# Performance work log

Hardware: AMD Instinct MI355X
Metric: run time of the kernel (lower is better)

Reference implementation:

```python
import jax, jax.numpy as jnp
import numpy as np

C = 4096
C8 = C // 8  # 512, must equal h*w
B, H, W = 32, 16, 32


def setup_inputs() -> dict:
    key = jax.random.key(0)
    ks = jax.random.split(key, 8)
    s = 0.02
    return {
        "x": jax.random.normal(ks[0], (B, C, H, W), dtype=jnp.float32),
        "Wq": jax.random.normal(ks[1], (C8, C), dtype=jnp.float32) * s,
        "bq": jax.random.normal(ks[2], (C8,), dtype=jnp.float32) * s,
        "Wk": jax.random.normal(ks[3], (C8, C), dtype=jnp.float32) * s,
        "bk": jax.random.normal(ks[4], (C8,), dtype=jnp.float32) * s,
        "Wv": jax.random.normal(ks[5], (C, C), dtype=jnp.float32) * s,
        "bv": jax.random.normal(ks[6], (C,), dtype=jnp.float32) * s,
        "gamma": jax.random.normal(ks[7], (1,), dtype=jnp.float32),
    }


def reference(x, Wq, bq, Wk, bk, Wv, bv, gamma):
    b, c, h, w = x.shape
    xf = x.reshape(b, c, h * w)               # (b, c, hw)
    # 1x1 conv == per-position linear over channels
    q = jnp.einsum("oc,bcl->bol", Wq, xf) + bq[None, :, None]   # (b, c8, hw)
    k = jnp.einsum("oc,bcl->bol", Wk, xf) + bk[None, :, None]   # (b, c8, hw)
    v = jnp.einsum("oc,bcl->bol", Wv, xf) + bv[None, :, None]   # (b, c, hw)
    # energy = bmm(Q, K^T): (b, c8, c8); no sqrt(d) scaling (faithful)
    energy = jnp.einsum("bol,bpl->bop", q, k)
    attn = jax.nn.softmax(energy, axis=-1)
    # out = bmm(V, attn^T): out[b,c,p] = sum_k V[b,c,k] * attn[b,p,k]
    out = jnp.einsum("bck,bpk->bcp", v, attn)  # requires hw == c8
    out = out.reshape(b, c, h, w)
    return gamma * out + x
```

## Files before the change

kernel.cpp:

```cpp
#include <hip/hip_runtime.h>


typedef _Float16 f16;
typedef _Float16 h8 __attribute__((ext_vector_type(8)));
typedef _Float16 h4 __attribute__((ext_vector_type(4)));
typedef _Float16 h2 __attribute__((ext_vector_type(2)));
typedef float fx4 __attribute__((ext_vector_type(4)));

#define CC  4096
#define C8  512
#define HWD 512
#define NB  32

__device__ __forceinline__ h8 ldfragC(const char* s, int row, int cb) {
  const int b = ((row << 7) | cb) ^ ((row & 7) << 4);
  return *reinterpret_cast<const h8*>(s + b);
}

#define AS1C(p) ((const __attribute__((address_space(1))) unsigned int*)(p))
#define AS3(p)  ((__attribute__((address_space(3))) unsigned int*)(p))


#define STAGE_ALL(bufsel) { \
  char* la_ = smem + ((bufsel) << 16); \
  char* lb_ = la_ + 32768; \
  _Pragma("unroll") for (int q = 0; q < 4; ++q) { \
    __builtin_amdgcn_global_load_lds(AS1C(pA[q]), AS3(la_ + (q << 13) + w1024), 16, 0, 0); \
    __builtin_amdgcn_global_load_lds(AS1C(pB[q]), AS3(lb_ + (q << 13) + w1024), 16, 0, 0); \
    pA[q] += 128; pB[q] += 128; } }

#define STAGE2(bufsel, q) { \
  char* la_ = smem + ((bufsel) << 16); \
  char* lb_ = la_ + 32768; \
  __builtin_amdgcn_global_load_lds(AS1C(pA[q]), AS3(la_ + ((q) << 13) + w1024), 16, 0, 0); \
  __builtin_amdgcn_global_load_lds(AS1C(pB[q]), AS3(lb_ + ((q) << 13) + w1024), 16, 0, 0); \
  pA[q] += 128; pB[q] += 128; }

#define DSREADS_A(dst, hm, kh) \
  _Pragma("unroll") for (int f = 0; f < 4; ++f) \
    dst[f] = ldfragC(At, wr * 128 + (hm) * 64 + f * 16 + frow, (kh) * 64 + kq);

#define DSREADS_B(dst, kh) \
  _Pragma("unroll") for (int g = 0; g < 4; ++g) \
    dst[g] = ldfragC(Bt, wc * 64 + g * 16 + frow, (kh) * 64 + kq);

#define MMA16(hm, av, bv) \
  __builtin_amdgcn_s_setprio(1); \
  _Pragma("unroll") for (int f = 0; f < 4; ++f) \
  _Pragma("unroll") for (int g = 0; g < 4; ++g) \
    acc[(hm) * 4 + f][g] = __builtin_amdgcn_mfma_f32_16x16x32_f16( \
        av[f], bv[g], acc[(hm) * 4 + f][g], 0, 0, 0); \
  __builtin_amdgcn_s_setprio(0);

#define KTILE(cur, DOSTAGE) { \
  const bool dost_ = (DOSTAGE); \
  const char* At = smem + ((cur) << 16); \
  const char* Bt = At + 32768; \
  h8 a0[4], a1[4], b0[4], b1[4]; \
  asm volatile("s_waitcnt vmcnt(0)" ::: "memory"); \
  __builtin_amdgcn_s_barrier(); \
   \
  DSREADS_A(a0, 0, 0) DSREADS_B(b0, 0) \
  if (dost_) { STAGE2((cur) ^ 1, 0) STAGE2((cur) ^ 1, 1) } \
  __builtin_amdgcn_s_barrier(); \
  asm volatile("s_waitcnt lgkmcnt(0)"); \
  MMA16(0, a0, b0) \
  __builtin_amdgcn_s_barrier(); \
   \
  DSREADS_A(a1, 1, 0) \
  if (dost_) { STAGE2((cur) ^ 1, 2) STAGE2((cur) ^ 1, 3) } \
  __builtin_amdgcn_s_barrier(); \
  asm volatile("s_waitcnt lgkmcnt(0)"); \
  MMA16(1, a1, b0) \
  __builtin_amdgcn_s_barrier(); \
   \
  DSREADS_A(a0, 0, 1) DSREADS_B(b1, 1) \
  __builtin_amdgcn_s_barrier(); \
  asm volatile("s_waitcnt lgkmcnt(0)"); \
  MMA16(0, a0, b1) \
  __builtin_amdgcn_s_barrier(); \
   \
  DSREADS_A(a1, 1, 1) \
  __builtin_amdgcn_s_barrier(); \
  asm volatile("s_waitcnt lgkmcnt(0)"); \
  MMA16(1, a1, b1) \
  __builtin_amdgcn_s_barrier(); \
}

template<int EPI>
__global__ __launch_bounds__(512, 2) void gemm256(
    const f16* __restrict__ Ah, const f16* __restrict__ Bh,
    int lda, int ldb, long sAb, long sBb, long sCb, int ldc, int K,
    const float* __restrict__ bias, float* __restrict__ Cf, f16* __restrict__ Ch,
    const float* __restrict__ resid, const float* __restrict__ gam)
{
  extern __shared__ __align__(16) char smem[];
  const int F  = blockIdx.x;
  const int Vv = ((F & 7) << 7) | (F >> 3);
  const int bz = Vv >> 5;
  const int m0 = (Vv & 15) << 8;
  const int n0 = ((Vv >> 4) & 1) << 8;

  const int T = threadIdx.x;
  const int lane = T & 63;
  const int w = T >> 6;
  const int wr = w >> 2, wc = w & 3;
  const int frow = lane & 15;
  const int kq = (lane >> 4) << 4;
  const int w1024 = w << 10;

  const int rr = T >> 3;
  const int corig = ((T & 7) << 4) ^ ((rr & 7) << 4);
  const char* pA[4];
  const char* pB[4];
#pragma unroll
  for (int q = 0; q < 4; ++q) {
    pA[q] = (const char*)(Ah + bz * sAb + (long)(m0 + q * 64 + rr) * lda) + corig;
    pB[q] = (const char*)(Bh + bz * sBb + (long)(n0 + q * 64 + rr) * ldb) + corig;
  }

  fx4 acc[8][4] = {};
  const int nt = K >> 6;

  STAGE_ALL(0)
  for (int t = 0; t < nt; t += 2) {
    KTILE(0, t + 1 < nt)
    KTILE(1, t + 2 < nt)
  }

  const int cm = (lane >> 4) << 2;
  const int cn = lane & 15;
  const float g0 = (EPI == 3) ? gam[0] : 0.f;
#pragma unroll
  for (int fm = 0; fm < 8; ++fm) {
    const int gr0 = m0 + wr * 128 + fm * 16 + cm;
#pragma unroll
    for (int fn = 0; fn < 4; ++fn) {
      const int gc = n0 + wc * 64 + fn * 16 + cn;
#pragma unroll
      for (int j = 0; j < 4; ++j) {
        const long ci = bz * sCb + (long)(gr0 + j) * ldc + gc;
        if constexpr (EPI == 1) Ch[ci] = (f16)(acc[fm][fn][j] + bias[gr0 + j]);
        else                    Cf[ci] = g0 * acc[fm][fn][j] + resid[ci];
      }
    }
  }
}

#define TSTG(p, off, ldB) { \
  _Pragma("unroll") for (int q = 0; q < 4; ++q) \
    __builtin_amdgcn_global_load_lds(AS1C((p) + (long)q * 32 * (ldB)), \
        AS3(smt + (off) + (q << 12) + (T << 4)), 16, 0, 0); \
  (p) += 128; }

template<int EPI>
__global__ __launch_bounds__(256) void gemm_tri(
    const f16* __restrict__ Ah, const f16* __restrict__ Al,
    const f16* __restrict__ Bh, const f16* __restrict__ Bl,
    int K, int lda, int ldb, long sAb, long sBb, long sCb, int ldc,
    const float* __restrict__ bias, const float* __restrict__ bias2,
    float* __restrict__ Cf, f16* __restrict__ Ch, f16* __restrict__ Cl)
{
  __shared__ __align__(16) char smt[65536];

  const int bz = blockIdx.z;
  const int m0 = blockIdx.y * 128, n0 = blockIdx.x * 128;
  const int T = threadIdx.x;
  const int lane = T & 63;
  const int wid  = T >> 6;
  const int wr = wid >> 1, wc = wid & 1;
  const int frow = lane & 15;
  const int kq = (lane >> 4) << 4;

  const int rr = T >> 3;
  const int cor = ((T & 7) << 4) ^ ((rr & 7) << 4);
  const long ldaB = (long)lda * 2, ldbB = (long)ldb * 2;
  const char* pAh = (const char*)(Ah + (long)bz * sAb + (long)(m0 + rr) * lda) + cor;
  const char* pAl = (const char*)(Al + (long)bz * sAb + (long)(m0 + rr) * lda) + cor;
  const char* pBh = (const char*)(Bh + (long)bz * sBb + (long)(n0 + rr) * ldb) + cor;
  const char* pBl = (const char*)(Bl + (long)bz * sBb + (long)(n0 + rr) * ldb) + cor;

  const char* sAh = smt;
  const char* sBh = smt + 16384;
  const char* sAl = smt + 32768;
  const char* sBl = smt + 49152;

  fx4 acc[4][4] = {};

  for (int k0 = 0; k0 < K; k0 += 64) {
    TSTG(pAh, 0, ldaB)
    TSTG(pBh, 16384, ldbB)
    TSTG(pAl, 32768, ldaB)
    TSTG(pBl, 49152, ldbB)
    asm volatile("s_waitcnt vmcnt(0)" ::: "memory");
    __syncthreads();
#pragma unroll
    for (int ks = 0; ks < 2; ++ks) {
      const int kb = ks * 64 + kq;
      h8 aH[4], bH[4], aL[4], bL[4];
#pragma unroll
      for (int f = 0; f < 4; ++f) {
        aH[f] = ldfragC(sAh, wr * 64 + f * 16 + frow, kb);
        bH[f] = ldfragC(sBh, wc * 64 + f * 16 + frow, kb);
        aL[f] = ldfragC(sAl, wr * 64 + f * 16 + frow, kb);
        bL[f] = ldfragC(sBl, wc * 64 + f * 16 + frow, kb);
      }
#pragma unroll
      for (int fm = 0; fm < 4; ++fm)
#pragma unroll
        for (int fn = 0; fn < 4; ++fn) {
          acc[fm][fn] = __builtin_amdgcn_mfma_f32_16x16x32_f16(aH[fm], bH[fn], acc[fm][fn], 0, 0, 0);
          acc[fm][fn] = __builtin_amdgcn_mfma_f32_16x16x32_f16(aH[fm], bL[fn], acc[fm][fn], 0, 0, 0);
          acc[fm][fn] = __builtin_amdgcn_mfma_f32_16x16x32_f16(aL[fm], bH[fn], acc[fm][fn], 0, 0, 0);
        }
    }
    __syncthreads();
  }

  const int cm = (lane >> 4) * 4;
  const int cn = lane & 15;
#pragma unroll
  for (int fm = 0; fm < 4; ++fm) {
    const int gr0 = m0 + wr * 64 + fm * 16 + cm;
#pragma unroll
    for (int fn = 0; fn < 4; ++fn) {
      const int gc = n0 + wc * 64 + fn * 16 + cn;
#pragma unroll
      for (int j = 0; j < 4; ++j) {
        const int gr = gr0 + j;
        const long ci = (long)bz * sCb + (long)gr * ldc + gc;
        float v = acc[fm][fn][j];
        if constexpr (EPI == 0) {
          v += (gr < 512) ? bias[gr] : bias2[gr - 512];
          const f16 h = (f16)v;
          Ch[ci] = h;
          Cl[ci] = (f16)(v - (float)h);
        } else {
          Cf[ci] = v;
        }
      }
    }
  }
}

__global__ void transpose_split_k(const float* __restrict__ x, f16* __restrict__ xh, f16* __restrict__ xl) {
  __shared__ float t[32][33];
  const int l0 = blockIdx.x * 32, c0 = blockIdx.y * 32;
  const long bi = (long)blockIdx.z * CC * HWD;
  const long bo = (long)blockIdx.z * HWD * CC;
  const int tx = threadIdx.x, ty = threadIdx.y;
#pragma unroll
  for (int i = 0; i < 2; ++i)
#pragma unroll
    for (int j = 0; j < 2; ++j)
      t[ty + 16 * i][tx + 16 * j] = x[bi + (long)(c0 + ty + 16 * i) * HWD + l0 + tx + 16 * j];
  __syncthreads();
#pragma unroll
  for (int i = 0; i < 2; ++i) {
    const int l = ty + 16 * i;
    const float v0 = t[2 * tx][l], v1 = t[2 * tx + 1][l];
    const f16 h0 = (f16)v0, h1 = (f16)v1;
    const long o = bo + (long)(l0 + l) * CC + c0 + 2 * tx;
    h2 hh; hh[0] = h0; hh[1] = h1;
    h2 ll; ll[0] = (f16)(v0 - (float)h0); ll[1] = (f16)(v1 - (float)h1);
    *reinterpret_cast<h2*>(xh + o) = hh;
    *reinterpret_cast<h2*>(xl + o) = ll;
  }
}

template<bool HASLO>
__global__ void split_k(const float* __restrict__ in, f16* __restrict__ hi, f16* __restrict__ lo, long n) {
  const long i = ((long)blockIdx.x * blockDim.x + threadIdx.x) * 4;
  if (i >= n) return;
  const float4 v = *reinterpret_cast<const float4*>(in + i);
  const float vv[4] = {v.x, v.y, v.z, v.w};
  h4 h, l;
#pragma unroll
  for (int j = 0; j < 4; ++j) {
    const f16 hh = (f16)vv[j];
    h[j] = hh;
    l[j] = (f16)(vv[j] - (float)hh);
  }
  *reinterpret_cast<h4*>(hi + i) = h;
  if constexpr (HASLO) *reinterpret_cast<h4*>(lo + i) = l;
}

__global__ __launch_bounds__(256) void softmax_k(const float* __restrict__ E, f16* __restrict__ attn) {
  const int lane = threadIdx.x & 63;
  const int wid  = threadIdx.x >> 6;
  const long row = (long)blockIdx.x * 4 + wid;
  const float* e = E + row * 512;
  const float4 a = *reinterpret_cast<const float4*>(e + lane * 8);
  const float4 b = *reinterpret_cast<const float4*>(e + lane * 8 + 4);
  float vv[8] = {a.x, a.y, a.z, a.w, b.x, b.y, b.z, b.w};
  float m = vv[0];
#pragma unroll
  for (int i = 1; i < 8; ++i) m = fmaxf(m, vv[i]);
#pragma unroll
  for (int s = 32; s > 0; s >>= 1) m = fmaxf(m, __shfl_xor(m, s));
  float sum = 0.f;
  float ex[8];
#pragma unroll
  for (int i = 0; i < 8; ++i) { ex[i] = __expf(vv[i] - m); sum += ex[i]; }
#pragma unroll
  for (int s = 32; s > 0; s >>= 1) sum += __shfl_xor(sum, s);
  const float inv = 1.f / sum;
  h8 o;
#pragma unroll
  for (int i = 0; i < 8; ++i) o[i] = (f16)(ex[i] * inv);
  *reinterpret_cast<h8*>(attn + row * 512 + lane * 8) = o;
}

extern "C" void kernel_launch(void* const* d_in, const int* in_sizes, int n_in,
                              void* d_out, int out_size, void* d_ws, size_t ws_size,
                              hipStream_t stream) {
  const float* x  = (const float*)d_in[0];
  const float* Wq = (const float*)d_in[1];
  const float* bq = (const float*)d_in[2];
  const float* Wk = (const float*)d_in[3];
  const float* bk = (const float*)d_in[4];
  const float* Wv = (const float*)d_in[5];
  const float* bv = (const float*)d_in[6];
  const float* gm = (const float*)d_in[7];
  float* out = (float*)d_out;

  const size_t szXT  = (size_t)NB * HWD * CC;
  const size_t szQK2 = (size_t)NB * 1024 * HWD;
  const size_t szW   = (size_t)C8 * CC;
  const size_t szWv  = (size_t)CC * CC;
  const size_t needBytes = (2 * szXT + 2 * szQK2 + 4 * szW + szWv) * sizeof(f16);
  if (ws_size < needBytes) return;

  f16* xT_h  = (f16*)d_ws;
  f16* xT_l  = xT_h + szXT;
  f16* v16   = xT_l;
  f16* qk_h  = xT_h + 2 * szXT;
  f16* qk_l  = qk_h + szQK2;
  f16* wqk_h = qk_l + szQK2;
  f16* wqk_l = wqk_h + 2 * szW;
  f16* attn  = wqk_h;
  f16* wv_h  = wqk_l + 2 * szW;
  float* E   = (float*)wv_h;

  split_k<true ><<<dim3((C8 * CC) / 1024), 256, 0, stream>>>(Wq, wqk_h, wqk_l, (long)C8 * CC);
  split_k<true ><<<dim3((C8 * CC) / 1024), 256, 0, stream>>>(Wk, wqk_h + szW, wqk_l + szW, (long)C8 * CC);
  split_k<false><<<dim3((CC * CC) / 1024), 256, 0, stream>>>(Wv, wv_h, nullptr, (long)CC * CC);
  transpose_split_k<<<dim3(HWD / 32, CC / 32, NB), dim3(16, 16), 0, stream>>>(x, xT_h, xT_l);
  gemm_tri<0><<<dim3(4, 8, NB), 256, 0, stream>>>(wqk_h, wqk_l, xT_h, xT_l, CC, CC, CC,
      0L, (long)HWD * CC, (long)1024 * HWD, HWD, bq, bk, nullptr, qk_h, qk_l);
  gemm256<1><<<dim3(1024), 512, 131072, stream>>>(wv_h, xT_h, CC, CC,
      0L, (long)HWD * CC, (long)CC * HWD, HWD, CC, bv, nullptr, v16, nullptr, nullptr);
  gemm_tri<2><<<dim3(4, 4, NB), 256, 0, stream>>>(qk_h, qk_l, qk_h + (size_t)512 * HWD, qk_l + (size_t)512 * HWD,
      HWD, HWD, HWD, (long)1024 * HWD, (long)1024 * HWD, (long)C8 * C8, C8,
      nullptr, nullptr, E, nullptr, nullptr);
  softmax_k<<<dim3(NB * C8 / 4), 256, 0, stream>>>(E, attn);
  gemm256<3><<<dim3(1024), 512, 131072, stream>>>(v16, attn, HWD, HWD,
      (long)CC * HWD, (long)C8 * HWD, (long)CC * HWD, HWD, C8, nullptr, out, nullptr, x, gm);
}
```

Baseline: 1.255 ms.

## Rewrite split-precision QK GEMM as double-buffered 512-thread pipelined kernel

Replaces the single-buffered 256-thread gemm_tri, which loaded a tile and then computed, with tri256. The new kernel uses 8 waves, a double-buffered 128KB dynamic LDS region and async global_load_lds prefetch of the next K tile interleaved with MFMA phases. It follows the same pattern as the existing gemm256 and adds a swizzled 1D block mapping across XCDs, with s_setprio around the MFMA bursts. The aim is to hide global load latency in the Q/K projection and energy GEMMs, at the cost of more LDS per block, which may reduce occupancy.

```diff
diff --git a/kernel.cpp b/kernel.cpp
--- a/kernel.cpp
+++ b/kernel.cpp
@@ -19,7 +19,6 @@
 
 #define AS1C(p) ((const __attribute__((address_space(1))) unsigned int*)(p))
 #define AS3(p)  ((__attribute__((address_space(3))) unsigned int*)(p))
-
 
 #define STAGE_ALL(bufsel) { \
   char* la_ = smem + ((bufsel) << 16); \
@@ -59,27 +58,23 @@
   h8 a0[4], a1[4], b0[4], b1[4]; \
   asm volatile("s_waitcnt vmcnt(0)" ::: "memory"); \
   __builtin_amdgcn_s_barrier(); \
-   \
   DSREADS_A(a0, 0, 0) DSREADS_B(b0, 0) \
   if (dost_) { STAGE2((cur) ^ 1, 0) STAGE2((cur) ^ 1, 1) } \
   __builtin_amdgcn_s_barrier(); \
   asm volatile("s_waitcnt lgkmcnt(0)"); \
   MMA16(0, a0, b0) \
   __builtin_amdgcn_s_barrier(); \
-   \
   DSREADS_A(a1, 1, 0) \
   if (dost_) { STAGE2((cur) ^ 1, 2) STAGE2((cur) ^ 1, 3) } \
   __builtin_amdgcn_s_barrier(); \
   asm volatile("s_waitcnt lgkmcnt(0)"); \
   MMA16(1, a1, b0) \
   __builtin_amdgcn_s_barrier(); \
-   \
   DSREADS_A(a0, 0, 1) DSREADS_B(b1, 1) \
   __builtin_amdgcn_s_barrier(); \
   asm volatile("s_waitcnt lgkmcnt(0)"); \
   MMA16(0, a0, b1) \
   __builtin_amdgcn_s_barrier(); \
-   \
   DSREADS_A(a1, 1, 1) \
   __builtin_amdgcn_s_barrier(); \
   asm volatile("s_waitcnt lgkmcnt(0)"); \
@@ -147,89 +142,129 @@
   }
 }
 
-#define TSTG(p, off, ldB) { \
-  _Pragma("unroll") for (int q = 0; q < 4; ++q) \
-    __builtin_amdgcn_global_load_lds(AS1C((p) + (long)q * 32 * (ldB)), \
-        AS3(smt + (off) + (q << 12) + (T << 4)), 16, 0, 0); \
-  (p) += 128; }
+
+#define TSTG(bufsel, i) { \
+  __builtin_amdgcn_global_load_lds(AS1C(pp[i]), \
+      AS3(smt + ((bufsel) << 16) + ((i) << 13) + (T << 4)), 16, 0, 0); \
+  pp[i] += 128; }
+
+#define TRD_A(dh, dl, mh, ks) { \
+  _Pragma("unroll") for (int f = 0; f < 2; ++f) { \
+    dh[f] = ldfragC(Aht, wr * 64 + (mh) * 32 + f * 16 + frow, (ks) * 64 + kq); \
+    dl[f] = ldfragC(Alt, wr * 64 + (mh) * 32 + f * 16 + frow, (ks) * 64 + kq); } }
+
+#define TRD_B(dh, dl, ks) { \
+  _Pragma("unroll") for (int g = 0; g < 2; ++g) { \
+    dh[g] = ldfragC(Bht, wc * 32 + g * 16 + frow, (ks) * 64 + kq); \
+    dl[g] = ldfragC(Blt, wc * 32 + g * 16 + frow, (ks) * 64 + kq); } }
+
+#define TMMA(mh, ah, al, bh, bl) \
+  __builtin_amdgcn_s_setprio(1); \
+  _Pragma("unroll") for (int f = 0; f < 2; ++f) \
+  _Pragma("unroll") for (int g = 0; g < 2; ++g) { \
+    acc[(mh) * 2 + f][g] = __builtin_amdgcn_mfma_f32_16x16x32_f16(ah[f], bh[g], acc[(mh) * 2 + f][g], 0, 0, 0); \
+    acc[(mh) * 2 + f][g] = __builtin_amdgcn_mfma_f32_16x16x32_f16(ah[f], bl[g], acc[(mh) * 2 + f][g], 0, 0, 0); \
+    acc[(mh) * 2 + f][g] = __builtin_amdgcn_mfma_f32_16x16x32_f16(al[f], bh[g], acc[(mh) * 2 + f][g], 0, 0, 0); } \
+  __builtin_amdgcn_s_setprio(0);
+
+#define KTILE_TRI(cur, dost) { \
+  const char* Aht = smt + ((cur) << 16); \
+  const char* Bht = Aht + 16384; \
+  const char* Alt = Aht + 32768; \
+  const char* Blt = Aht + 49152; \
+  h8 xah[2], xal[2], xbh[2], xbl[2], yah[2], yal[2]; \
+  asm volatile("s_waitcnt vmcnt(0)" ::: "memory"); \
+  __builtin_amdgcn_s_barrier(); \
+   \
+  TRD_A(xah, xal, 0, 0) TRD_B(xbh, xbl, 0) \
+  if (dost) { TSTG((cur) ^ 1, 0) TSTG((cur) ^ 1, 1) TSTG((cur) ^ 1, 2) TSTG((cur) ^ 1, 3) } \
+  __builtin_amdgcn_s_barrier(); \
+  asm volatile("s_waitcnt lgkmcnt(0)"); \
+  TMMA(0, xah, xal, xbh, xbl) \
+  __builtin_amdgcn_s_barrier(); \
+   \
+  TRD_A(yah, yal, 1, 0) \
+  if (dost) { TSTG((cur) ^ 1, 4) TSTG((cur) ^ 1, 5) TSTG((cur) ^ 1, 6) TSTG((cur) ^ 1, 7) } \
+  __builtin_amdgcn_s_barrier(); \
+  asm volatile("s_waitcnt lgkmcnt(0)"); \
+  TMMA(1, yah, yal, xbh, xbl) \
+  __builtin_amdgcn_s_barrier(); \
+   \
+  TRD_A(xah, xal, 0, 1) TRD_B(xbh, xbl, 1) \
+  __builtin_amdgcn_s_barrier(); \
+  asm volatile("s_waitcnt lgkmcnt(0)"); \
+  TMMA(0, xah, xal, xbh, xbl) \
+  __builtin_amdgcn_s_barrier(); \
+   \
+  TRD_A(yah, yal, 1, 1) \
+  __builtin_amdgcn_s_barrier(); \
+  asm volatile("s_waitcnt lgkmcnt(0)"); \
+  TMMA(1, yah, yal, xbh, xbl) \
+  __builtin_amdgcn_s_barrier(); \
+}
 
 template<int EPI>
-__global__ __launch_bounds__(256) void gemm_tri(
+__global__ __launch_bounds__(512, 2) void tri256(
     const f16* __restrict__ Ah, const f16* __restrict__ Al,
     const f16* __restrict__ Bh, const f16* __restrict__ Bl,
     int K, int lda, int ldb, long sAb, long sBb, long sCb, int ldc,
+    int nm, int nn,
     const float* __restrict__ bias, const float* __restrict__ bias2,
     float* __restrict__ Cf, f16* __restrict__ Ch, f16* __restrict__ Cl)
 {
-  __shared__ __align__(16) char smt[65536];
-
-  const int bz = blockIdx.z;
-  const int m0 = blockIdx.y * 128, n0 = blockIdx.x * 128;
+  extern __shared__ __align__(16) char smt[];
+  const int F = blockIdx.x;
+  const int chunk = gridDim.x >> 3;
+  const int Vv = (F & 7) * chunk + (F >> 3);
+  const int mi = Vv % nm;
+  const int r2 = Vv / nm;
+  const int ni = r2 % nn;
+  const int bz = r2 / nn;
+  const int m0 = mi << 7, n0 = ni << 7;
+
   const int T = threadIdx.x;
   const int lane = T & 63;
-  const int wid  = T >> 6;
-  const int wr = wid >> 1, wc = wid & 1;
+  const int w = T >> 6;
+  const int wr = w >> 2, wc = w & 3;
   const int frow = lane & 15;
   const int kq = (lane >> 4) << 4;
 
   const int rr = T >> 3;
-  const int cor = ((T & 7) << 4) ^ ((rr & 7) << 4);
-  const long ldaB = (long)lda * 2, ldbB = (long)ldb * 2;
-  const char* pAh = (const char*)(Ah + (long)bz * sAb + (long)(m0 + rr) * lda) + cor;
-  const char* pAl = (const char*)(Al + (long)bz * sAb + (long)(m0 + rr) * lda) + cor;
-  const char* pBh = (const char*)(Bh + (long)bz * sBb + (long)(n0 + rr) * ldb) + cor;
-  const char* pBl = (const char*)(Bl + (long)bz * sBb + (long)(n0 + rr) * ldb) + cor;
-
-  const char* sAh = smt;
-  const char* sBh = smt + 16384;
-  const char* sAl = smt + 32768;
-  const char* sBl = smt + 49152;
-
-  fx4 acc[4][4] = {};
-
-  for (int k0 = 0; k0 < K; k0 += 64) {
-    TSTG(pAh, 0, ldaB)
-    TSTG(pBh, 16384, ldbB)
-    TSTG(pAl, 32768, ldaB)
-    TSTG(pBl, 49152, ldbB)
-    asm volatile("s_waitcnt vmcnt(0)" ::: "memory");
-    __syncthreads();
-#pragma unroll
-    for (int ks = 0; ks < 2; ++ks) {
-      const int kb = ks * 64 + kq;
-      h8 aH[4], bH[4], aL[4], bL[4];
-#pragma unroll
-      for (int f = 0; f < 4; ++f) {
-        aH[f] = ldfragC(sAh, wr * 64 + f * 16 + frow, kb);
-        bH[f] = ldfragC(sBh, wc * 64 + f * 16 + frow, kb);
-        aL[f] = ldfragC(sAl, wr * 64 + f * 16 + frow, kb);
-        bL[f] = ldfragC(sBl, wc * 64 + f * 16 + frow, kb);
-      }
-#pragma unroll
-      for (int fm = 0; fm < 4; ++fm)
-#pragma unroll
-        for (int fn = 0; fn < 4; ++fn) {
-          acc[fm][fn] = __builtin_amdgcn_mfma_f32_16x16x32_f16(aH[fm], bH[fn], acc[fm][fn], 0, 0, 0);
-          acc[fm][fn] = __builtin_amdgcn_mfma_f32_16x16x32_f16(aH[fm], bL[fn], acc[fm][fn], 0, 0, 0);
-          acc[fm][fn] = __builtin_amdgcn_mfma_f32_16x16x32_f16(aL[fm], bH[fn], acc[fm][fn], 0, 0, 0);
-        }
-    }
-    __syncthreads();
-  }
-
-  const int cm = (lane >> 4) * 4;
+  const int corig = ((T & 7) << 4) ^ ((rr & 7) << 4);
+  const char* pp[8];
+#pragma unroll
+  for (int q = 0; q < 2; ++q) {
+    pp[0 + q] = (const char*)(Ah + bz * sAb + (long)(m0 + q * 64 + rr) * lda) + corig;
+    pp[2 + q] = (const char*)(Bh + bz * sBb + (long)(n0 + q * 64 + rr) * ldb) + corig;
+    pp[4 + q] = (const char*)(Al + bz * sAb + (long)(m0 + q * 64 + rr) * lda) + corig;
+    pp[6 + q] = (const char*)(Bl + bz * sBb + (long)(n0 + q * 64 + rr) * ldb) + corig;
+  }
+
+  fx4 acc[4][2] = {};
+  const int nt = K >> 6;
+
+#pragma unroll
+  for (int i = 0; i < 8; ++i) TSTG(0, i)
+  for (int t = 0; t < nt; t += 2) {
+    KTILE_TRI(0, t + 1 < nt)
+    KTILE_TRI(1, t + 2 < nt)
+  }
+
+  const int cm = (lane >> 4) << 2;
   const int cn = lane & 15;
 #pragma unroll
-  for (int fm = 0; fm < 4; ++fm) {
-    const int gr0 = m0 + wr * 64 + fm * 16 + cm;
-#pragma unroll
-    for (int fn = 0; fn < 4; ++fn) {
-      const int gc = n0 + wc * 64 + fn * 16 + cn;
+  for (int mh = 0; mh < 2; ++mh)
+#pragma unroll
+  for (int f = 0; f < 2; ++f) {
+    const int gr0 = m0 + wr * 64 + mh * 32 + f * 16 + cm;
+#pragma unroll
+    for (int g = 0; g < 2; ++g) {
+      const int gc = n0 + wc * 32 + g * 16 + cn;
 #pragma unroll
       for (int j = 0; j < 4; ++j) {
         const int gr = gr0 + j;
         const long ci = (long)bz * sCb + (long)gr * ldc + gc;
-        float v = acc[fm][fn][j];
+        float v = acc[mh * 2 + f][g][j];
         if constexpr (EPI == 0) {
           v += (gr < 512) ? bias[gr] : bias2[gr - 512];
           const f16 h = (f16)v;
@@ -346,13 +381,14 @@
   split_k<true ><<<dim3((C8 * CC) / 1024), 256, 0, stream>>>(Wk, wqk_h + szW, wqk_l + szW, (long)C8 * CC);
   split_k<false><<<dim3((CC * CC) / 1024), 256, 0, stream>>>(Wv, wv_h, nullptr, (long)CC * CC);
   transpose_split_k<<<dim3(HWD / 32, CC / 32, NB), dim3(16, 16), 0, stream>>>(x, xT_h, xT_l);
-  gemm_tri<0><<<dim3(4, 8, NB), 256, 0, stream>>>(wqk_h, wqk_l, xT_h, xT_l, CC, CC, CC,
-      0L, (long)HWD * CC, (long)1024 * HWD, HWD, bq, bk, nullptr, qk_h, qk_l);
+  tri256<0><<<dim3(1024), 512, 131072, stream>>>(wqk_h, wqk_l, xT_h, xT_l, CC, CC, CC,
+      0L, (long)HWD * CC, (long)1024 * HWD, HWD, 8, 4, bq, bk, nullptr, qk_h, qk_l);
   gemm256<1><<<dim3(1024), 512, 131072, stream>>>(wv_h, xT_h, CC, CC,
       0L, (long)HWD * CC, (long)CC * HWD, HWD, CC, bv, nullptr, v16, nullptr, nullptr);
-  gemm_tri<2><<<dim3(4, 4, NB), 256, 0, stream>>>(qk_h, qk_l, qk_h + (size_t)512 * HWD, qk_l + (size_t)512 * HWD,
+  tri256<2><<<dim3(512), 512, 131072, stream>>>(qk_h, qk_l,
+      qk_h + (size_t)512 * HWD, qk_l + (size_t)512 * HWD,
       HWD, HWD, HWD, (long)1024 * HWD, (long)1024 * HWD, (long)C8 * C8, C8,
-      nullptr, nullptr, E, nullptr, nullptr);
+      4, 4, nullptr, nullptr, E, nullptr, nullptr);
   softmax_k<<<dim3(NB * C8 / 4), 256, 0, stream>>>(E, attn);
   gemm256<3><<<dim3(1024), 512, 131072, stream>>>(v16, attn, HWD, HWD,
       (long)CC * HWD, (long)C8 * HWD, (long)CC * HWD, HWD, C8, nullptr, out, nullptr, x, gm);
```

Result: no change. 1.279 ms (+1.9%).

## Software-pipeline LDS fragment reads one quarter ahead of MFMA in GEMM k-loop

Applied to the files above, without the earlier changes.

Restructures the k-tile loop so the LDS fragment reads for the next MFMA quarter are issued before the current quarter's MFMAs. Partial lgkmcnt waits and sched_barriers replace the full waits, and each tile drops from eight barriers to four. The first fragments of the next tile are prefetched at the end of the current one, with a prologue and peeled epilogue. This hides LDS read latency behind matrix math, at the cost of extra live registers and hand-tuned wait counts that must match the issued reads.

```diff
diff --git a/kernel.cpp b/kernel.cpp
--- a/kernel.cpp
+++ b/kernel.cpp
@@ -36,55 +36,58 @@
   __builtin_amdgcn_global_load_lds(AS1C(pB[q]), AS3(lb_ + ((q) << 13) + w1024), 16, 0, 0); \
   pA[q] += 128; pB[q] += 128; }
 
-#define DSREADS_A(dst, hm, kh) \
+#define RD_A(dst, mh, kh, base) { \
   _Pragma("unroll") for (int f = 0; f < 4; ++f) \
-    dst[f] = ldfragC(At, wr * 128 + (hm) * 64 + f * 16 + frow, (kh) * 64 + kq);
-
-#define DSREADS_B(dst, kh) \
+    dst[f] = ldfragC(base, wr * 128 + (mh) * 64 + f * 16 + frow, (kh) * 64 + kq); }
+
+#define RD_B(dst, kh, base) { \
   _Pragma("unroll") for (int g = 0; g < 4; ++g) \
-    dst[g] = ldfragC(Bt, wc * 64 + g * 16 + frow, (kh) * 64 + kq);
-
-#define MMA16(hm, av, bv) \
+    dst[g] = ldfragC(base, wc * 64 + g * 16 + frow, (kh) * 64 + kq); }
+
+#define MMAQ(mh, av, bv) { \
   __builtin_amdgcn_s_setprio(1); \
   _Pragma("unroll") for (int f = 0; f < 4; ++f) \
   _Pragma("unroll") for (int g = 0; g < 4; ++g) \
-    acc[(hm) * 4 + f][g] = __builtin_amdgcn_mfma_f32_16x16x32_f16( \
-        av[f], bv[g], acc[(hm) * 4 + f][g], 0, 0, 0); \
-  __builtin_amdgcn_s_setprio(0);
-
-#define KTILE(cur, DOSTAGE) { \
-  const bool dost_ = (DOSTAGE); \
+    acc[(mh) * 4 + f][g] = __builtin_amdgcn_mfma_f32_16x16x32_f16( \
+        av[f], bv[g], acc[(mh) * 4 + f][g], 0, 0, 0); \
+  __builtin_amdgcn_s_setprio(0); }
+
+#define KTILE(cur, dost, dolast) { \
   const char* At = smem + ((cur) << 16); \
   const char* Bt = At + 32768; \
-  h8 a0[4], a1[4], b0[4], b1[4]; \
+  const char* An = smem + (((cur) ^ 1) << 16); \
+  const char* Bn = An + 32768; \
+   \
+  __builtin_amdgcn_s_barrier(); \
+  RD_A(a1, 1, 0, At) \
+  if (dost) { STAGE2((cur) ^ 1, 0) STAGE2((cur) ^ 1, 1) } \
+  asm volatile("s_waitcnt lgkmcnt(4)"); \
+  __builtin_amdgcn_sched_barrier(0); \
+  MMAQ(0, a0, bb0) \
+   \
+  __builtin_amdgcn_s_barrier(); \
+  RD_A(a0, 0, 1, At) RD_B(bb1, 1, Bt) \
+  if (dost) { STAGE2((cur) ^ 1, 2) STAGE2((cur) ^ 1, 3) } \
+  asm volatile("s_waitcnt lgkmcnt(8)"); \
+  __builtin_amdgcn_sched_barrier(0); \
+  MMAQ(1, a1, bb0) \
+   \
+  __builtin_amdgcn_s_barrier(); \
+  RD_A(a1, 1, 1, At) \
+  asm volatile("s_waitcnt lgkmcnt(4)"); \
+  __builtin_amdgcn_sched_barrier(0); \
+  MMAQ(0, a0, bb1) \
+   \
   asm volatile("s_waitcnt vmcnt(0)" ::: "memory"); \
   __builtin_amdgcn_s_barrier(); \
-   \
-  DSREADS_A(a0, 0, 0) DSREADS_B(b0, 0) \
-  if (dost_) { STAGE2((cur) ^ 1, 0) STAGE2((cur) ^ 1, 1) } \
-  __builtin_amdgcn_s_barrier(); \
-  asm volatile("s_waitcnt lgkmcnt(0)"); \
-  MMA16(0, a0, b0) \
-  __builtin_amdgcn_s_barrier(); \
-   \
-  DSREADS_A(a1, 1, 0) \
-  if (dost_) { STAGE2((cur) ^ 1, 2) STAGE2((cur) ^ 1, 3) } \
-  __builtin_amdgcn_s_barrier(); \
-  asm volatile("s_waitcnt lgkmcnt(0)"); \
-  MMA16(1, a1, b0) \
-  __builtin_amdgcn_s_barrier(); \
-   \
-  DSREADS_A(a0, 0, 1) DSREADS_B(b1, 1) \
-  __builtin_amdgcn_s_barrier(); \
-  asm volatile("s_waitcnt lgkmcnt(0)"); \
-  MMA16(0, a0, b1) \
-  __builtin_amdgcn_s_barrier(); \
-   \
-  DSREADS_A(a1, 1, 1) \
-  __builtin_amdgcn_s_barrier(); \
-  asm volatile("s_waitcnt lgkmcnt(0)"); \
-  MMA16(1, a1, b1) \
-  __builtin_amdgcn_s_barrier(); \
+  if (!(dolast)) { \
+    RD_A(a0, 0, 0, An) RD_B(bb0, 0, Bn) \
+    asm volatile("s_waitcnt lgkmcnt(8)"); \
+  } else { \
+    asm volatile("s_waitcnt lgkmcnt(0)"); \
+  } \
+  __builtin_amdgcn_sched_barrier(0); \
+  MMAQ(1, a1, bb1) \
 }
 
 template<int EPI>
@@ -120,13 +123,20 @@
   }
 
   fx4 acc[8][4] = {};
+  h8 a0[4], a1[4], bb0[4], bb1[4];
   const int nt = K >> 6;
 
   STAGE_ALL(0)
-  for (int t = 0; t < nt; t += 2) {
-    KTILE(0, t + 1 < nt)
-    KTILE(1, t + 2 < nt)
-  }
+  asm volatile("s_waitcnt vmcnt(0)" ::: "memory");
+  __builtin_amdgcn_s_barrier();
+  RD_A(a0, 0, 0, smem) RD_B(bb0, 0, smem + 32768)
+
+  for (int t = 0; t + 2 < nt; t += 2) {
+    KTILE(0, 1, 0)
+    KTILE(1, 1, 0)
+  }
+  KTILE(0, 1, 0)
+  KTILE(1, 0, 1)
 
   const int cm = (lane >> 4) << 2;
   const int cn = lane & 15;
```

Result: slower. 1.381 ms (+10.1%).

## Halve GEMM K-tile to 32 and shrink LDS to fit two blocks per CU

Applied to the files above, without the earlier changes.

The main 256x256 GEMM now stages 32-wide K slices instead of 64, with a new swizzled LDS layout and fragment loader, and drops the second half of the per-tile MMA phases. Shared memory per block falls from 128KB to 64KB, so two blocks can reside on a CU and overlap each other's memory and barrier stalls. The cost is twice as many synchronization rounds per unit of K, and less MMA work between each barrier.

```diff
diff --git a/kernel.cpp b/kernel.cpp
--- a/kernel.cpp
+++ b/kernel.cpp
@@ -17,32 +17,32 @@
   return *reinterpret_cast<const h8*>(s + b);
 }
 
+__device__ __forceinline__ h8 ldfrag32(const char* s, int row, int kc) {
+  const int chunk = ((row >> 7) << 2) | kc;
+  const int b = ((row & 127) << 7) | ((chunk ^ (row & 7)) << 4);
+  return *reinterpret_cast<const h8*>(s + b);
+}
+
 #define AS1C(p) ((const __attribute__((address_space(1))) unsigned int*)(p))
 #define AS3(p)  ((__attribute__((address_space(3))) unsigned int*)(p))
 
 
-#define STAGE_ALL(bufsel) { \
-  char* la_ = smem + ((bufsel) << 16); \
-  char* lb_ = la_ + 32768; \
-  _Pragma("unroll") for (int q = 0; q < 4; ++q) { \
-    __builtin_amdgcn_global_load_lds(AS1C(pA[q]), AS3(la_ + (q << 13) + w1024), 16, 0, 0); \
-    __builtin_amdgcn_global_load_lds(AS1C(pB[q]), AS3(lb_ + (q << 13) + w1024), 16, 0, 0); \
-    pA[q] += 128; pB[q] += 128; } }
-
-#define STAGE2(bufsel, q) { \
-  char* la_ = smem + ((bufsel) << 16); \
-  char* lb_ = la_ + 32768; \
-  __builtin_amdgcn_global_load_lds(AS1C(pA[q]), AS3(la_ + ((q) << 13) + w1024), 16, 0, 0); \
-  __builtin_amdgcn_global_load_lds(AS1C(pB[q]), AS3(lb_ + ((q) << 13) + w1024), 16, 0, 0); \
-  pA[q] += 128; pB[q] += 128; }
-
-#define DSREADS_A(dst, hm, kh) \
+#define STGA32(bufsel, q) { \
+  __builtin_amdgcn_global_load_lds(AS1C(pA[q]), \
+      AS3(smem + ((bufsel) << 15) + ((q) << 13) + (T << 4)), 16, 0, 0); \
+  pA[q] += 64; }
+#define STGB32(bufsel, q) { \
+  __builtin_amdgcn_global_load_lds(AS1C(pB[q]), \
+      AS3(smem + ((bufsel) << 15) + 16384 + ((q) << 13) + (T << 4)), 16, 0, 0); \
+  pB[q] += 64; }
+
+#define RD_A32(dst, mh) { \
   _Pragma("unroll") for (int f = 0; f < 4; ++f) \
-    dst[f] = ldfragC(At, wr * 128 + (hm) * 64 + f * 16 + frow, (kh) * 64 + kq);
-
-#define DSREADS_B(dst, kh) \
+    dst[f] = ldfrag32(At, wr * 128 + (mh) * 64 + f * 16 + frow, kc); }
+
+#define RD_B32(dst) { \
   _Pragma("unroll") for (int g = 0; g < 4; ++g) \
-    dst[g] = ldfragC(Bt, wc * 64 + g * 16 + frow, (kh) * 64 + kq);
+    dst[g] = ldfrag32(Bt, wc * 64 + g * 16 + frow, kc); }
 
 #define MMA16(hm, av, bv) \
   __builtin_amdgcn_s_setprio(1); \
@@ -52,38 +52,26 @@
         av[f], bv[g], acc[(hm) * 4 + f][g], 0, 0, 0); \
   __builtin_amdgcn_s_setprio(0);
 
-#define KTILE(cur, DOSTAGE) { \
+#define KTILE32(cur, DOSTAGE) { \
   const bool dost_ = (DOSTAGE); \
-  const char* At = smem + ((cur) << 16); \
-  const char* Bt = At + 32768; \
-  h8 a0[4], a1[4], b0[4], b1[4]; \
+  const char* At = smem + ((cur) << 15); \
+  const char* Bt = At + 16384; \
+  h8 a0[4], a1[4], b0[4]; \
   asm volatile("s_waitcnt vmcnt(0)" ::: "memory"); \
   __builtin_amdgcn_s_barrier(); \
    \
-  DSREADS_A(a0, 0, 0) DSREADS_B(b0, 0) \
-  if (dost_) { STAGE2((cur) ^ 1, 0) STAGE2((cur) ^ 1, 1) } \
+  RD_A32(a0, 0) RD_B32(b0) \
+  if (dost_) { STGA32((cur) ^ 1, 0) STGB32((cur) ^ 1, 0) } \
   __builtin_amdgcn_s_barrier(); \
   asm volatile("s_waitcnt lgkmcnt(0)"); \
   MMA16(0, a0, b0) \
   __builtin_amdgcn_s_barrier(); \
    \
-  DSREADS_A(a1, 1, 0) \
-  if (dost_) { STAGE2((cur) ^ 1, 2) STAGE2((cur) ^ 1, 3) } \
+  RD_A32(a1, 1) \
+  if (dost_) { STGA32((cur) ^ 1, 1) STGB32((cur) ^ 1, 1) } \
   __builtin_amdgcn_s_barrier(); \
   asm volatile("s_waitcnt lgkmcnt(0)"); \
   MMA16(1, a1, b0) \
-  __builtin_amdgcn_s_barrier(); \
-   \
-  DSREADS_A(a0, 0, 1) DSREADS_B(b1, 1) \
-  __builtin_amdgcn_s_barrier(); \
-  asm volatile("s_waitcnt lgkmcnt(0)"); \
-  MMA16(0, a0, b1) \
-  __builtin_amdgcn_s_barrier(); \
-   \
-  DSREADS_A(a1, 1, 1) \
-  __builtin_amdgcn_s_barrier(); \
-  asm volatile("s_waitcnt lgkmcnt(0)"); \
-  MMA16(1, a1, b1) \
   __builtin_amdgcn_s_barrier(); \
 }
 
@@ -106,26 +94,26 @@
   const int w = T >> 6;
   const int wr = w >> 2, wc = w & 3;
   const int frow = lane & 15;
-  const int kq = (lane >> 4) << 4;
-  const int w1024 = w << 10;
-
-  const int rr = T >> 3;
-  const int corig = ((T & 7) << 4) ^ ((rr & 7) << 4);
-  const char* pA[4];
-  const char* pB[4];
-#pragma unroll
-  for (int q = 0; q < 4; ++q) {
-    pA[q] = (const char*)(Ah + bz * sAb + (long)(m0 + q * 64 + rr) * lda) + corig;
-    pB[q] = (const char*)(Bh + bz * sBb + (long)(n0 + q * 64 + rr) * ldb) + corig;
+  const int kc = lane >> 4;
+
+  const int Rl = (T >> 3) & 7;
+  const int corig = (T & 7) ^ Rl;
+  const char* pA[2];
+  const char* pB[2];
+#pragma unroll
+  for (int q = 0; q < 2; ++q) {
+    const int tr = q * 64 + (T >> 3) + ((corig >> 2) << 7);
+    pA[q] = (const char*)(Ah + bz * sAb + (long)(m0 + tr) * lda) + (corig & 3) * 16;
+    pB[q] = (const char*)(Bh + bz * sBb + (long)(n0 + tr) * ldb) + (corig & 3) * 16;
   }
 
   fx4 acc[8][4] = {};
-  const int nt = K >> 6;
-
-  STAGE_ALL(0)
+  const int nt = K >> 5;
+
+  STGA32(0, 0) STGA32(0, 1) STGB32(0, 0) STGB32(0, 1)
   for (int t = 0; t < nt; t += 2) {
-    KTILE(0, t + 1 < nt)
-    KTILE(1, t + 2 < nt)
+    KTILE32(0, t + 1 < nt)
+    KTILE32(1, t + 2 < nt)
   }
 
   const int cm = (lane >> 4) << 2;
@@ -348,12 +336,12 @@
   transpose_split_k<<<dim3(HWD / 32, CC / 32, NB), dim3(16, 16), 0, stream>>>(x, xT_h, xT_l);
   gemm_tri<0><<<dim3(4, 8, NB), 256, 0, stream>>>(wqk_h, wqk_l, xT_h, xT_l, CC, CC, CC,
       0L, (long)HWD * CC, (long)1024 * HWD, HWD, bq, bk, nullptr, qk_h, qk_l);
-  gemm256<1><<<dim3(1024), 512, 131072, stream>>>(wv_h, xT_h, CC, CC,
+  gemm256<1><<<dim3(1024), 512, 65536, stream>>>(wv_h, xT_h, CC, CC,
       0L, (long)HWD * CC, (long)CC * HWD, HWD, CC, bv, nullptr, v16, nullptr, nullptr);
   gemm_tri<2><<<dim3(4, 4, NB), 256, 0, stream>>>(qk_h, qk_l, qk_h + (size_t)512 * HWD, qk_l + (size_t)512 * HWD,
       HWD, HWD, HWD, (long)1024 * HWD, (long)1024 * HWD, (long)C8 * C8, C8,
       nullptr, nullptr, E, nullptr, nullptr);
   softmax_k<<<dim3(NB * C8 / 4), 256, 0, stream>>>(E, attn);
-  gemm256<3><<<dim3(1024), 512, 131072, stream>>>(v16, attn, HWD, HWD,
+  gemm256<3><<<dim3(1024), 512, 65536, stream>>>(v16, attn, HWD, HWD,
       (long)CC * HWD, (long)C8 * HWD, (long)CC * HWD, HWD, C8, nullptr, out, nullptr, x, gm);
 }
```

Measured after the change: 1.338 ms. 1.07x slower.
